# Kernel tuning notes

Measured on AMD Instinct MI355X. Metric: run time of the kernel, lower is better.

## Reference

```python
import jax, jax.numpy as jnp
import numpy as np

T = 64
LAMBDA_SCALE = 4
RECON = 512
U = 2 ** (LAMBDA_SCALE - 1)          # 8
YT = RECON // U                      # 64
P = YT * YT                          # 4096


def convert_Ht2Weights(Ht, u):
    # Ht: [T, recon, recon] -> per-low-res-pixel weights [P, T, u*u]
    t, r, _ = Ht.shape
    yt = r // u
    w = Ht.reshape(t, yt, u, yt, u)
    w = jnp.transpose(w, (1, 3, 0, 2, 4))        # [yt, yt, T, u, u]
    return w.reshape(yt * yt, t, u * u)


def setup_inputs() -> dict:
    key = jax.random.key(0)
    k1, k2, k3 = jax.random.split(key, 3)
    yt = jax.random.normal(k1, (64, T, YT, YT), dtype=jnp.float32)
    Ht = jax.random.normal(k2, (T, RECON, RECON), dtype=jnp.float32)
    biases = jax.random.normal(k3, (P, 1, U * U), dtype=jnp.float32)
    return {"yt": yt, "Ht": Ht, "biases": biases}


def reference(yt, Ht, biases):
    B = yt.shape[0]
    # [B, T, yt, yt] -> [P, B, T]
    y = yt.reshape(B, T, P).transpose(2, 0, 1)
    weights = convert_Ht2Weights(Ht, U)          # [P, T, u*u]
    # per-pixel batched GEMM + bias
    up = jnp.einsum('pbt,ptu->pbu', y, weights) + biases   # [P, B, u*u]
    # pixel-shuffle back to full resolution
    up = up.reshape(YT, YT, B, U, U)
    up = jnp.transpose(up, (2, 0, 3, 1, 4)).reshape(B, RECON, RECON)
    return up[:, None]                            # [B, 1, recon, recon] (seq_block = identity)
```

## Files before the change

### kernel.cpp

```cpp
#include <hip/hip_runtime.h>

typedef float f32x4 __attribute__((ext_vector_type(4)));
typedef short s16x8 __attribute__((ext_vector_type(8)));
typedef unsigned int u32;

__device__ __forceinline__ u32 f2bf(float x) {
    u32 u = __float_as_uint(x);
    return (u + 0x7FFFu + ((u >> 16) & 1u)) >> 16;
}
__device__ __forceinline__ u32 pk(float a, float b) {
    return f2bf(a) | (f2bf(b) << 16);
}

__global__ __launch_bounds__(256, 2)
void upsample_mfma_kernel(const float* __restrict__ yt,
                          const float* __restrict__ Ht,
                          const float* __restrict__ biases,
                          float* __restrict__ out)
{
    __shared__ __align__(16) unsigned short Al[16 * 776];
    __shared__ __align__(16) unsigned short Wl[16 * 1544];

    const int wg = blockIdx.x;
    const int nw  = (wg & 7) * 64 + (wg >> 3);
    const int py  = nw >> 3;
    const int pxq = (nw >> 1) & 3;
    const int bh  = nw & 1;
    const int px0 = pxq * 16;
    const int b0  = bh * 32;
    const int tid = (int)threadIdx.x;

    const int a_pxg = tid & 3;
    const int a_bb  = (tid >> 2) & 31;
    const int a_tg  = tid >> 7;
    const float* a_base = yt + (size_t)(b0 + a_bb) * 262144 + py * 64 + px0 + a_pxg * 4;

    const int w_cc = tid & 31;
    const int w_uy = tid >> 5;
    const float* w_base = Ht + (size_t)(py * 8 + w_uy) * 512 + pxq * 128 + w_cc * 4;
    const int w_px  = w_cc >> 1;
    const int w_uu0 = w_uy * 8 + (w_cc & 1) * 4;

    const int wv = tid >> 6;
    const int l  = tid & 63;
    const int r  = l & 15;
    const int q  = l >> 4;
    const bool qlo = (q < 2);
    const int qq = (q & 1) * 8;

    f32x4 acc[4][2][4];
    #pragma unroll
    for (int pxi = 0; pxi < 4; ++pxi) {
        const int p = py * 64 + px0 + wv * 4 + pxi;
        #pragma unroll
        for (int nb = 0; nb < 4; ++nb) {
            const float bv = biases[p * 64 + nb * 16 + r];
            #pragma unroll
            for (int mb = 0; mb < 2; ++mb)
                acc[pxi][mb][nb] = (f32x4){bv, bv, bv, bv};
        }
    }

    const s16x8 zz = (s16x8){0, 0, 0, 0, 0, 0, 0, 0};

    #pragma unroll
    for (int tt = 0; tt < 4; ++tt) {
        const int t0 = tt * 16;
        if (tt) __syncthreads();

        {
            f32x4 v[8];
            #pragma unroll
            for (int j = 0; j < 8; ++j)
                v[j] = *(const f32x4*)(a_base + (size_t)(t0 + a_tg * 8 + j) * 4096);
            #pragma unroll
            for (int i = 0; i < 4; ++i) {
                uint4 g;
                g.x = pk(v[0][i], v[1][i]);
                g.y = pk(v[2][i], v[3][i]);
                g.z = pk(v[4][i], v[5][i]);
                g.w = pk(v[6][i], v[7][i]);
                *(uint4*)&Al[(a_pxg * 4 + i) * 776 + a_bb * 24 + a_tg * 8] = g;
            }
        }
        #pragma unroll
        for (int h = 0; h < 2; ++h) {
            f32x4 v[8];
            #pragma unroll
            for (int j = 0; j < 8; ++j)
                v[j] = *(const f32x4*)(w_base + (size_t)(t0 + h * 8 + j) * 262144);
            #pragma unroll
            for (int i = 0; i < 4; ++i) {
                uint4 g;
                g.x = pk(v[0][i], v[1][i]);
                g.y = pk(v[2][i], v[3][i]);
                g.z = pk(v[4][i], v[5][i]);
                g.w = pk(v[6][i], v[7][i]);
                *(uint4*)&Wl[w_px * 1544 + (w_uu0 + i) * 24 + h * 8] = g;
            }
        }
        __syncthreads();

        #pragma unroll
        for (int pxi = 0; pxi < 4; ++pxi) {
            const unsigned short* ap = &Al[(wv * 4 + pxi) * 776];
            const unsigned short* wp = &Wl[(wv * 4 + pxi) * 1544];
            s16x8 af[2], bfr[4];
            #pragma unroll
            for (int mb = 0; mb < 2; ++mb)
                af[mb] = qlo ? *(const s16x8*)&ap[(mb * 16 + r) * 24 + qq] : zz;
            #pragma unroll
            for (int nb = 0; nb < 4; ++nb)
                bfr[nb] = qlo ? *(const s16x8*)&wp[(nb * 16 + r) * 24 + qq] : zz;
            #pragma unroll
            for (int mb = 0; mb < 2; ++mb)
                #pragma unroll
                for (int nb = 0; nb < 4; ++nb)
                    acc[pxi][mb][nb] = __builtin_amdgcn_mfma_f32_16x16x32_bf16(
                        af[mb], bfr[nb], acc[pxi][mb][nb], 0, 0, 0);
        }
    }

    #pragma unroll
    for (int pxi = 0; pxi < 4; ++pxi) {
        const int px = px0 + wv * 4 + pxi;
        #pragma unroll
        for (int mb = 0; mb < 2; ++mb) {
            #pragma unroll
            for (int nb = 0; nb < 4; ++nb) {
                const int n   = nb * 16 + r;
                const int row = py * 8 + (n >> 3);
                const int col = px * 8 + (n & 7);
                #pragma unroll
                for (int i = 0; i < 4; ++i) {
                    const int b = b0 + mb * 16 + q * 4 + i;
                    out[(size_t)(b * 512 + row) * 512 + col] = acc[pxi][mb][nb][i];
                }
            }
        }
    }
}

extern "C" void kernel_launch(void* const* d_in, const int* in_sizes, int n_in,
                              void* d_out, int out_size, void* d_ws, size_t ws_size,
                              hipStream_t stream) {
    const float* yt     = (const float*)d_in[0];
    const float* Ht     = (const float*)d_in[1];
    const float* biases = (const float*)d_in[2];
    float* out          = (float*)d_out;
    upsample_mfma_kernel<<<dim3(512), dim3(256), 0, stream>>>(yt, Ht, biases, out);
}
```

Measured before the change: 40.57 us.

## Keep full-T weight tile resident and loop over both batch halves per block

Each block now loads the whole 64-step weight slice for its 16 pixels into a swizzled LDS buffer once and reuses it for both 32-batch halves. Before, two blocks each reloaded and converted the same weights. The grid halves to 256 blocks of 512 threads, and activation tiles are prefetched into registers one step ahead of the MFMA work. The swizzle is meant to avoid LDS bank conflicts on the larger weight buffer. In exchange, block count and per-block parallelism drop, LDS use rises, and there are more barriers per block.

```diff
diff --git a/kernel.cpp b/kernel.cpp
--- a/kernel.cpp
+++ b/kernel.cpp
@@ -11,132 +11,154 @@
 __device__ __forceinline__ u32 pk(float a, float b) {
     return f2bf(a) | (f2bf(b) << 16);
 }
+__device__ __forceinline__ int swzW(int row, int t) {
+    int g = ((row ^ (row >> 3)) & 7) << 3;
+    return row * 64 + (t ^ g);
+}
 
-__global__ __launch_bounds__(256, 2)
+__global__ __launch_bounds__(512, 2)
 void upsample_mfma_kernel(const float* __restrict__ yt,
                           const float* __restrict__ Ht,
                           const float* __restrict__ biases,
                           float* __restrict__ out)
 {
-    __shared__ __align__(16) unsigned short Al[16 * 776];
-    __shared__ __align__(16) unsigned short Wl[16 * 1544];
+    __shared__ __align__(16) unsigned short Wl[16 * 4104];
+    __shared__ __align__(16) unsigned short Al[16 * 768];
 
-    const int wg = blockIdx.x;
-    const int nw  = (wg & 7) * 64 + (wg >> 3);
-    const int py  = nw >> 3;
-    const int pxq = (nw >> 1) & 3;
-    const int bh  = nw & 1;
+    const int wg  = blockIdx.x;
+    const int nw  = (wg & 7) * 32 + (wg >> 3);
+    const int py  = nw >> 2;
+    const int pxq = nw & 3;
     const int px0 = pxq * 16;
-    const int b0  = bh * 32;
     const int tid = (int)threadIdx.x;
 
     const int a_pxg = tid & 3;
-    const int a_bb  = (tid >> 2) & 31;
+    const int a_b   = (tid >> 2) & 31;
     const int a_tg  = tid >> 7;
-    const float* a_base = yt + (size_t)(b0 + a_bb) * 262144 + py * 64 + px0 + a_pxg * 4;
+    const float* a_base = yt + (size_t)a_b * 262144 + (size_t)py * 64 + px0
+                        + a_pxg * 4 + (size_t)a_tg * 4 * 4096;
 
     const int w_cc = tid & 31;
-    const int w_uy = tid >> 5;
-    const float* w_base = Ht + (size_t)(py * 8 + w_uy) * 512 + pxq * 128 + w_cc * 4;
+    const int w_uy = (tid >> 5) & 7;
+    const int w_th = tid >> 8;
+    const float* w_base = Ht + ((size_t)py * 8 + w_uy) * 512 + pxq * 128 + w_cc * 4;
     const int w_px  = w_cc >> 1;
     const int w_uu0 = w_uy * 8 + (w_cc & 1) * 4;
 
     const int wv = tid >> 6;
-    const int l  = tid & 63;
-    const int r  = l & 15;
-    const int q  = l >> 4;
+    const int l = tid & 63, r = l & 15, q = l >> 4;
     const bool qlo = (q < 2);
     const int qq = (q & 1) * 8;
+    const s16x8 zz = (s16x8){0, 0, 0, 0, 0, 0, 0, 0};
 
-    f32x4 acc[4][2][4];
+    f32x4 v[4];
     #pragma unroll
-    for (int pxi = 0; pxi < 4; ++pxi) {
-        const int p = py * 64 + px0 + wv * 4 + pxi;
+    for (int j = 0; j < 4; ++j)
+        v[j] = *(const f32x4*)(a_base + (size_t)j * 4096);
+
+    #pragma unroll
+    for (int rr = 0; rr < 4; ++rr) {
+        const int t0 = rr * 16 + w_th * 8;
+        f32x4 wv8[8];
         #pragma unroll
-        for (int nb = 0; nb < 4; ++nb) {
-            const float bv = biases[p * 64 + nb * 16 + r];
-            #pragma unroll
-            for (int mb = 0; mb < 2; ++mb)
-                acc[pxi][mb][nb] = (f32x4){bv, bv, bv, bv};
+        for (int j = 0; j < 8; ++j)
+            wv8[j] = *(const f32x4*)(w_base + (size_t)(t0 + j) * 262144);
+        #pragma unroll
+        for (int i = 0; i < 4; ++i) {
+            uint4 g;
+            g.x = pk(wv8[0][i], wv8[1][i]);
+            g.y = pk(wv8[2][i], wv8[3][i]);
+            g.z = pk(wv8[4][i], wv8[5][i]);
+            g.w = pk(wv8[6][i], wv8[7][i]);
+            *(uint4*)&Wl[w_px * 4104 + swzW(w_uu0 + i, t0)] = g;
         }
     }
+    #pragma unroll
+    for (int i = 0; i < 4; ++i)
+        *(uint2*)&Al[(a_pxg * 4 + i) * 768 + a_b * 24 + a_tg * 4] =
+            make_uint2(pk(v[0][i], v[1][i]), pk(v[2][i], v[3][i]));
 
-    const s16x8 zz = (s16x8){0, 0, 0, 0, 0, 0, 0, 0};
+    float bv[2][4];
+    #pragma unroll
+    for (int pxi = 0; pxi < 2; ++pxi) {
+        const int p = py * 64 + px0 + wv * 2 + pxi;
+        #pragma unroll
+        for (int nb = 0; nb < 4; ++nb)
+            bv[pxi][nb] = biases[p * 64 + nb * 16 + r];
+    }
+    f32x4 acc[2][2][4];
+    #pragma unroll
+    for (int pxi = 0; pxi < 2; ++pxi)
+        #pragma unroll
+        for (int mb = 0; mb < 2; ++mb)
+            #pragma unroll
+            for (int nb = 0; nb < 4; ++nb)
+                acc[pxi][mb][nb] = (f32x4){bv[pxi][nb], bv[pxi][nb], bv[pxi][nb], bv[pxi][nb]};
+
+    __syncthreads();
 
     #pragma unroll
-    for (int tt = 0; tt < 4; ++tt) {
-        const int t0 = tt * 16;
-        if (tt) __syncthreads();
+    for (int i = 0; i < 8; ++i) {
+        const int bh = i >> 2, tt = i & 3;
 
-        {
-            f32x4 v[8];
+        if (i < 7) {
+            const int ni = i + 1;
+            const float* ab = a_base + (size_t)(ni >> 2) * 32 * 262144
+                                     + (size_t)(ni & 3) * 16 * 4096;
             #pragma unroll
-            for (int j = 0; j < 8; ++j)
-                v[j] = *(const f32x4*)(a_base + (size_t)(t0 + a_tg * 8 + j) * 4096);
-            #pragma unroll
-            for (int i = 0; i < 4; ++i) {
-                uint4 g;
-                g.x = pk(v[0][i], v[1][i]);
-                g.y = pk(v[2][i], v[3][i]);
-                g.z = pk(v[4][i], v[5][i]);
-                g.w = pk(v[6][i], v[7][i]);
-                *(uint4*)&Al[(a_pxg * 4 + i) * 776 + a_bb * 24 + a_tg * 8] = g;
-            }
+            for (int j = 0; j < 4; ++j)
+                v[j] = *(const f32x4*)(ab + (size_t)j * 4096);
         }
-        #pragma unroll
-        for (int h = 0; h < 2; ++h) {
-            f32x4 v[8];
-            #pragma unroll
-            for (int j = 0; j < 8; ++j)
-                v[j] = *(const f32x4*)(w_base + (size_t)(t0 + h * 8 + j) * 262144);
-            #pragma unroll
-            for (int i = 0; i < 4; ++i) {
-                uint4 g;
-                g.x = pk(v[0][i], v[1][i]);
-                g.y = pk(v[2][i], v[3][i]);
-                g.z = pk(v[4][i], v[5][i]);
-                g.w = pk(v[6][i], v[7][i]);
-                *(uint4*)&Wl[w_px * 1544 + (w_uu0 + i) * 24 + h * 8] = g;
-            }
-        }
-        __syncthreads();
 
         #pragma unroll
-        for (int pxi = 0; pxi < 4; ++pxi) {
-            const unsigned short* ap = &Al[(wv * 4 + pxi) * 776];
-            const unsigned short* wp = &Wl[(wv * 4 + pxi) * 1544];
-            s16x8 af[2], bfr[4];
+        for (int pxi = 0; pxi < 2; ++pxi) {
+            const unsigned short* ap = &Al[(wv * 2 + pxi) * 768];
+            const unsigned short* wp = &Wl[(wv * 2 + pxi) * 4104];
+            s16x8 af[2], bf[4];
             #pragma unroll
             for (int mb = 0; mb < 2; ++mb)
                 af[mb] = qlo ? *(const s16x8*)&ap[(mb * 16 + r) * 24 + qq] : zz;
             #pragma unroll
             for (int nb = 0; nb < 4; ++nb)
-                bfr[nb] = qlo ? *(const s16x8*)&wp[(nb * 16 + r) * 24 + qq] : zz;
+                bf[nb] = qlo ? *(const s16x8*)&wp[swzW(nb * 16 + r, tt * 16 + qq)] : zz;
             #pragma unroll
             for (int mb = 0; mb < 2; ++mb)
                 #pragma unroll
                 for (int nb = 0; nb < 4; ++nb)
                     acc[pxi][mb][nb] = __builtin_amdgcn_mfma_f32_16x16x32_bf16(
-                        af[mb], bfr[nb], acc[pxi][mb][nb], 0, 0, 0);
+                        af[mb], bf[nb], acc[pxi][mb][nb], 0, 0, 0);
         }
-    }
 
-    #pragma unroll
-    for (int pxi = 0; pxi < 4; ++pxi) {
-        const int px = px0 + wv * 4 + pxi;
-        #pragma unroll
-        for (int mb = 0; mb < 2; ++mb) {
+        if (tt == 3) {
             #pragma unroll
-            for (int nb = 0; nb < 4; ++nb) {
-                const int n   = nb * 16 + r;
-                const int row = py * 8 + (n >> 3);
-                const int col = px * 8 + (n & 7);
+            for (int pxi = 0; pxi < 2; ++pxi) {
+                const int px = px0 + wv * 2 + pxi;
                 #pragma unroll
-                for (int i = 0; i < 4; ++i) {
-                    const int b = b0 + mb * 16 + q * 4 + i;
-                    out[(size_t)(b * 512 + row) * 512 + col] = acc[pxi][mb][nb][i];
+                for (int mb = 0; mb < 2; ++mb) {
+                    #pragma unroll
+                    for (int nb = 0; nb < 4; ++nb) {
+                        const int n   = nb * 16 + r;
+                        const int row = py * 8 + (n >> 3);
+                        const int col = px * 8 + (n & 7);
+                        float* ob = out + ((size_t)(bh * 32 + mb * 16 + q * 4) * 512 + row) * 512 + col;
+                        #pragma unroll
+                        for (int ii = 0; ii < 4; ++ii)
+                            ob[(size_t)ii * 262144] = acc[pxi][mb][nb][ii];
+                        if (bh == 0)
+                            acc[pxi][mb][nb] = (f32x4){bv[pxi][nb], bv[pxi][nb],
+                                                       bv[pxi][nb], bv[pxi][nb]};
+                    }
                 }
             }
+        }
+
+        __syncthreads();
+        if (i < 7) {
+            #pragma unroll
+            for (int ii = 0; ii < 4; ++ii)
+                *(uint2*)&Al[(a_pxg * 4 + ii) * 768 + a_b * 24 + a_tg * 4] =
+                    make_uint2(pk(v[0][ii], v[1][ii]), pk(v[2][ii], v[3][ii]));
+            __syncthreads();
         }
     }
 }
@@ -148,5 +170,5 @@
     const float* Ht     = (const float*)d_in[1];
     const float* biases = (const float*)d_in[2];
     float* out          = (float*)d_out;
-    upsample_mfma_kernel<<<dim3(512), dim3(256), 0, stream>>>(yt, Ht, biases, out);
+    upsample_mfma_kernel<<<dim3(256), dim3(512), 0, stream>>>(yt, Ht, biases, out);
 }
```

After: 40.79 us. Within noise of the previous version (+0.6%).

## Restructure tiling to 8 pixels × 64 batches with full-K MFMA and swizzled LDS

Applied to the files above, without the earlier changes.

Each workgroup now covers 8 low-res pixels and all 64 batches, with 512 threads, one wave per pixel. Weight fragments for the full T=64 are loaded once into registers, so each weight is fetched from global memory only once per pixel. The old layout zeroed half of each MFMA operand (qlo) and so used only half of K; the new code fills all K=32 slots, halving the MFMA count. LDS now uses an XOR swizzle instead of padding to avoid bank conflicts, at the cost of larger workgroups and higher register pressure.

```diff
diff --git a/kernel.cpp b/kernel.cpp
--- a/kernel.cpp
+++ b/kernel.cpp
@@ -11,68 +11,84 @@
 __device__ __forceinline__ u32 pk(float a, float b) {
     return f2bf(a) | (f2bf(b) << 16);
 }
+__device__ __forceinline__ int swz(int row, int t) {
+    int g = ((row ^ (row >> 3)) & 7) << 3;
+    return row * 64 + (t ^ g);
+}
 
-__global__ __launch_bounds__(256, 2)
+__global__ __launch_bounds__(512, 4)
 void upsample_mfma_kernel(const float* __restrict__ yt,
                           const float* __restrict__ Ht,
                           const float* __restrict__ biases,
                           float* __restrict__ out)
 {
-    __shared__ __align__(16) unsigned short Al[16 * 776];
-    __shared__ __align__(16) unsigned short Wl[16 * 1544];
+    __shared__ __align__(16) unsigned short S[32768];
 
-    const int wg = blockIdx.x;
-    const int nw  = (wg & 7) * 64 + (wg >> 3);
-    const int py  = nw >> 3;
-    const int pxq = (nw >> 1) & 3;
-    const int bh  = nw & 1;
-    const int px0 = pxq * 16;
-    const int b0  = bh * 32;
+    const int wg  = blockIdx.x;
+    const int py  = (wg & 7) + ((wg >> 3) & 7) * 8;
+    const int pxo = wg >> 6;
+    const int px0 = pxo * 8;
     const int tid = (int)threadIdx.x;
 
-    const int a_pxg = tid & 3;
-    const int a_bb  = (tid >> 2) & 31;
-    const int a_tg  = tid >> 7;
-    const float* a_base = yt + (size_t)(b0 + a_bb) * 262144 + py * 64 + px0 + a_pxg * 4;
-
-    const int w_cc = tid & 31;
-    const int w_uy = tid >> 5;
-    const float* w_base = Ht + (size_t)(py * 8 + w_uy) * 512 + pxq * 128 + w_cc * 4;
-    const int w_px  = w_cc >> 1;
-    const int w_uu0 = w_uy * 8 + (w_cc & 1) * 4;
+    {
+        const int c4 = tid & 15;
+        const int uy = (tid >> 4) & 7;
+        const int tq = tid >> 7;
+        const float* wb = Ht + (size_t)(py * 8 + uy) * 512 + px0 * 8 + c4 * 4;
+        #pragma unroll
+        for (int ph = 0; ph < 2; ++ph) {
+            const int t0 = ph * 32 + tq * 8;
+            f32x4 v[8];
+            #pragma unroll
+            for (int k = 0; k < 8; ++k)
+                v[k] = *(const f32x4*)(wb + (size_t)(t0 + k) * 262144);
+            #pragma unroll
+            for (int cc = 0; cc < 4; ++cc) {
+                const int c   = c4 * 4 + cc;
+                const int pxl = c >> 3;
+                const int uu  = uy * 8 + (c & 7);
+                uint4 g;
+                g.x = pk(v[0][cc], v[1][cc]);
+                g.y = pk(v[2][cc], v[3][cc]);
+                g.z = pk(v[4][cc], v[5][cc]);
+                g.w = pk(v[6][cc], v[7][cc]);
+                *(uint4*)&S[pxl * 4096 + swz(uu, t0)] = g;
+            }
+        }
+    }
+    __syncthreads();
 
     const int wv = tid >> 6;
-    const int l  = tid & 63;
-    const int r  = l & 15;
-    const int q  = l >> 4;
-    const bool qlo = (q < 2);
-    const int qq = (q & 1) * 8;
+    const int l = tid & 63, r = l & 15, q = l >> 4;
+    s16x8 wf[4][2];
+    #pragma unroll
+    for (int nb = 0; nb < 4; ++nb)
+        #pragma unroll
+        for (int ks = 0; ks < 2; ++ks)
+            wf[nb][ks] = *(const s16x8*)&S[wv * 4096 + swz(nb * 16 + r, ks * 32 + q * 8)];
 
-    f32x4 acc[4][2][4];
+    const int px = px0 + wv;
+    const int p  = py * 64 + px;
+    float bv[4];
     #pragma unroll
-    for (int pxi = 0; pxi < 4; ++pxi) {
-        const int p = py * 64 + px0 + wv * 4 + pxi;
+    for (int nb = 0; nb < 4; ++nb)
+        bv[nb] = biases[(size_t)p * 64 + nb * 16 + r];
+
+    __syncthreads();
+
+    {
+        const int pxh = tid & 1;
+        const int ab  = (tid >> 1) & 31;
+        const int atq = tid >> 6;
+        const float* abase = yt + (size_t)py * 64 + px0 + pxh * 4
+                           + (size_t)atq * 8 * 4096;
         #pragma unroll
-        for (int nb = 0; nb < 4; ++nb) {
-            const float bv = biases[p * 64 + nb * 16 + r];
-            #pragma unroll
-            for (int mb = 0; mb < 2; ++mb)
-                acc[pxi][mb][nb] = (f32x4){bv, bv, bv, bv};
-        }
-    }
-
-    const s16x8 zz = (s16x8){0, 0, 0, 0, 0, 0, 0, 0};
-
-    #pragma unroll
-    for (int tt = 0; tt < 4; ++tt) {
-        const int t0 = tt * 16;
-        if (tt) __syncthreads();
-
-        {
+        for (int bc = 0; bc < 2; ++bc) {
+            const float* ap = abase + (size_t)(bc * 32 + ab) * 262144;
             f32x4 v[8];
             #pragma unroll
-            for (int j = 0; j < 8; ++j)
-                v[j] = *(const f32x4*)(a_base + (size_t)(t0 + a_tg * 8 + j) * 4096);
+            for (int k = 0; k < 8; ++k)
+                v[k] = *(const f32x4*)(ap + (size_t)k * 4096);
             #pragma unroll
             for (int i = 0; i < 4; ++i) {
                 uint4 g;
@@ -80,50 +96,36 @@
                 g.y = pk(v[2][i], v[3][i]);
                 g.z = pk(v[4][i], v[5][i]);
                 g.w = pk(v[6][i], v[7][i]);
-                *(uint4*)&Al[(a_pxg * 4 + i) * 776 + a_bb * 24 + a_tg * 8] = g;
+                *(uint4*)&S[bc * 16384 + (pxh * 4 + i) * 2048 + swz(ab, atq * 8)] = g;
             }
         }
+    }
+    __syncthreads();
+
+    #pragma unroll
+    for (int bc = 0; bc < 2; ++bc) {
+        f32x4 acc[2][4];
         #pragma unroll
-        for (int h = 0; h < 2; ++h) {
-            f32x4 v[8];
+        for (int mb = 0; mb < 2; ++mb)
             #pragma unroll
-            for (int j = 0; j < 8; ++j)
-                v[j] = *(const f32x4*)(w_base + (size_t)(t0 + h * 8 + j) * 262144);
-            #pragma unroll
-            for (int i = 0; i < 4; ++i) {
-                uint4 g;
-                g.x = pk(v[0][i], v[1][i]);
-                g.y = pk(v[2][i], v[3][i]);
-                g.z = pk(v[4][i], v[5][i]);
-                g.w = pk(v[6][i], v[7][i]);
-                *(uint4*)&Wl[w_px * 1544 + (w_uu0 + i) * 24 + h * 8] = g;
-            }
-        }
-        __syncthreads();
+            for (int nb = 0; nb < 4; ++nb)
+                acc[mb][nb] = (f32x4){bv[nb], bv[nb], bv[nb], bv[nb]};
 
         #pragma unroll
-        for (int pxi = 0; pxi < 4; ++pxi) {
-            const unsigned short* ap = &Al[(wv * 4 + pxi) * 776];
-            const unsigned short* wp = &Wl[(wv * 4 + pxi) * 1544];
-            s16x8 af[2], bfr[4];
+        for (int ks = 0; ks < 2; ++ks) {
+            s16x8 af[2];
             #pragma unroll
             for (int mb = 0; mb < 2; ++mb)
-                af[mb] = qlo ? *(const s16x8*)&ap[(mb * 16 + r) * 24 + qq] : zz;
-            #pragma unroll
-            for (int nb = 0; nb < 4; ++nb)
-                bfr[nb] = qlo ? *(const s16x8*)&wp[(nb * 16 + r) * 24 + qq] : zz;
+                af[mb] = *(const s16x8*)&S[bc * 16384 + wv * 2048
+                                           + swz(mb * 16 + r, ks * 32 + q * 8)];
             #pragma unroll
             for (int mb = 0; mb < 2; ++mb)
                 #pragma unroll
                 for (int nb = 0; nb < 4; ++nb)
-                    acc[pxi][mb][nb] = __builtin_amdgcn_mfma_f32_16x16x32_bf16(
-                        af[mb], bfr[nb], acc[pxi][mb][nb], 0, 0, 0);
+                    acc[mb][nb] = __builtin_amdgcn_mfma_f32_16x16x32_bf16(
+                        af[mb], wf[nb][ks], acc[mb][nb], 0, 0, 0);
         }
-    }
 
-    #pragma unroll
-    for (int pxi = 0; pxi < 4; ++pxi) {
-        const int px = px0 + wv * 4 + pxi;
         #pragma unroll
         for (int mb = 0; mb < 2; ++mb) {
             #pragma unroll
@@ -131,11 +133,10 @@
                 const int n   = nb * 16 + r;
                 const int row = py * 8 + (n >> 3);
                 const int col = px * 8 + (n & 7);
+                float* ob = out + ((size_t)(bc * 32 + mb * 16 + q * 4) * 512 + row) * 512 + col;
                 #pragma unroll
-                for (int i = 0; i < 4; ++i) {
-                    const int b = b0 + mb * 16 + q * 4 + i;
-                    out[(size_t)(b * 512 + row) * 512 + col] = acc[pxi][mb][nb][i];
-                }
+                for (int ii = 0; ii < 4; ++ii)
+                    ob[(size_t)ii * 262144] = acc[mb][nb][ii];
             }
         }
     }
@@ -148,5 +149,5 @@
     const float* Ht     = (const float*)d_in[1];
     const float* biases = (const float*)d_in[2];
     float* out          = (float*)d_out;
-    upsample_mfma_kernel<<<dim3(512), dim3(256), 0, stream>>>(yt, Ht, biases, out);
+    upsample_mfma_kernel<<<dim3(512), dim3(512), 0, stream>>>(yt, Ht, biases, out);
 }
```

New measurement: 39.99 us. About the same (-1.4%).
